# Kernel tuning notes

Measured on AMD Instinct MI355X. Metric: run time of the kernel, lower is better.

Reference implementation:

```python
import jax, jax.numpy as jnp
import numpy as np

VOCAB = 50257
EMBED = 256
UNITS = 1024   # dec_units == attention units == GRU units
ENC_D = 1024   # encoder feature dim
B = 64
T_ENC = 128


def setup_inputs() -> dict:
    key = jax.random.key(0)
    ks = jax.random.split(key, 16)
    s = lambda k, *sh: jax.random.normal(k, sh, dtype=jnp.float32) * 0.02
    gru_in = ENC_D + EMBED  # concat(context, embedding)
    return {
        "x": jax.random.randint(ks[0], (B, 1), 0, VOCAB),
        "hidden": jax.random.normal(ks[1], (B, UNITS), dtype=jnp.float32),
        "enc_output": jax.random.normal(ks[2], (B, T_ENC, ENC_D), dtype=jnp.float32),
        "emb": s(ks[3], VOCAB, EMBED),
        "W1": s(ks[4], UNITS, UNITS), "b1": jnp.zeros((UNITS,), jnp.float32),
        "W2": s(ks[5], ENC_D, UNITS), "b2": jnp.zeros((UNITS,), jnp.float32),
        "V": s(ks[6], UNITS, 1), "bV": jnp.zeros((1,), jnp.float32),
        "gru_kernel": s(ks[7], gru_in, 3 * UNITS),
        "gru_rkernel": s(ks[8], UNITS, 3 * UNITS),
        "gru_bias": jnp.zeros((2, 3 * UNITS), jnp.float32),  # reset_after=True: [input_bias, recurrent_bias]
        "fcW": s(ks[9], UNITS, VOCAB), "fcb": jnp.zeros((VOCAB,), jnp.float32),
    }


def reference(x, hidden, enc_output, emb, W1, b1, W2, b2, V, bV,
              gru_kernel, gru_rkernel, gru_bias, fcW, fcb):
    # --- Bahdanau attention ---
    q = hidden[:, None, :] @ W1 + b1                    # [B,1,U]
    k = enc_output @ W2 + b2                            # [B,T,U]
    score = jnp.tanh(q + k) @ V + bV                    # [B,T,1]
    attw = jax.nn.softmax(score, axis=1)                # [B,T,1]
    context = jnp.sum(attw * enc_output, axis=1)        # [B,ENC_D]

    # --- embed token and concat (single time step) ---
    e = emb[x[:, 0]]                                    # [B,EMBED]
    xin = jnp.concatenate([context, e], axis=-1)        # [B,ENC_D+EMBED]

    # --- single GRU step (keras default reset_after=True), initial state zeros
    # (original code calls self.gru(x) without initial_state) ---
    h0 = jnp.zeros((xin.shape[0], UNITS), xin.dtype)
    xz, xr, xh = jnp.split(xin @ gru_kernel + gru_bias[0], 3, axis=-1)
    rz, rr, rh = jnp.split(h0 @ gru_rkernel + gru_bias[1], 3, axis=-1)
    z = jax.nn.sigmoid(xz + rz)
    r = jax.nn.sigmoid(xr + rr)
    hh = jnp.tanh(xh + r * rh)
    h = z * h0 + (1.0 - z) * hh                          # [B,U]

    logits = h @ fcW + fcb                               # [B,VOCAB]
    return logits, h, attw
```

## Files before the change

kernel.cpp:

```cpp
#include <hip/hip_runtime.h>
#include <hip/hip_bf16.h>

#define UNITS 1024
#define EMBED 256
#define TENC  128
#define BATCH 64
#define VOCAB 50257
#define GRU_IN 1280
#define MROWS 8192
#define NCB   8
#define NSPLIT 8

typedef __bf16 bf16x8 __attribute__((ext_vector_type(8)));
typedef float  f32x4  __attribute__((ext_vector_type(4)));
typedef float  f32x4u __attribute__((ext_vector_type(4), aligned(4)));

__device__ __forceinline__ void gload_lds16(const void* gsrc, void* ldst) {
  __builtin_amdgcn_global_load_lds(
      (const __attribute__((address_space(1))) void*)gsrc,
      (__attribute__((address_space(3))) void*)ldst,
      16, 0, 0);
}

__global__ __launch_bounds__(256) void convert_kernel(
    const float* __restrict__ enc, const float* __restrict__ W2,
    __bf16* __restrict__ encb, __bf16* __restrict__ w2t)
{
  __shared__ __bf16 tl[64][72];
  const int bid = blockIdx.x;
  const int tid = threadIdx.x;
  if (bid < 4096) {
    const size_t base = ((size_t)bid * 256 + tid) * 8;
    const f32x4 v0 = *reinterpret_cast<const f32x4*>(enc + base);
    const f32x4 v1 = *reinterpret_cast<const f32x4*>(enc + base + 4);
    bf16x8 o;
#pragma unroll
    for (int j = 0; j < 4; ++j) { o[j] = (__bf16)v0[j]; o[4 + j] = (__bf16)v1[j]; }
    *reinterpret_cast<bf16x8*>(encb + base) = o;
  } else {
    const int ti  = bid - 4096;
    const int kt0 = (ti >> 4) * 64, nt0 = (ti & 15) * 64;
    const int r = tid >> 2, q = (tid & 3) * 16;
    const float* wp = W2 + (size_t)(kt0 + r) * UNITS + nt0 + q;
#pragma unroll
    for (int v = 0; v < 4; ++v) {
      const f32x4 a = *reinterpret_cast<const f32x4*>(wp + v * 4);
#pragma unroll
      for (int j = 0; j < 4; ++j) tl[r][q + v * 4 + j] = (__bf16)a[j];
    }
    __syncthreads();
    const int n = tid >> 2, kq = (tid & 3) * 16;
    bf16x8 o0, o1;
#pragma unroll
    for (int j = 0; j < 8; ++j) { o0[j] = tl[kq + j][n]; o1[j] = tl[kq + 8 + j][n]; }
    __bf16* op = w2t + (size_t)(nt0 + n) * UNITS + kt0 + kq;
    *reinterpret_cast<bf16x8*>(op)     = o0;
    *reinterpret_cast<bf16x8*>(op + 8) = o1;
  }
}

__global__ __launch_bounds__(256) void gemm_splitk(
    const float* __restrict__ A, const float* __restrict__ B,
    float* __restrict__ Cpart, int M, int N, int K, int Kc)
{
  const int col0  = blockIdx.y * 64;
  const int kbase = blockIdx.z * Kc;
  const int tid  = threadIdx.x;
  const int lane = tid & 63;
  const int wid  = tid >> 6;
  const int wm   = (wid >> 1) * 32;
  const int wn   = (wid & 1) * 32;

  __shared__ __bf16 As[2][4][64][8];
  __shared__ __bf16 Bs[2][4][64][8];

  f32x4 acc[2][2] = {};

  const int ar  = tid >> 2;
  const int akc = (tid & 3) * 8;
  const int bkk = tid >> 4;
  const int bn  = (tid & 15) * 4;

  f32x4 pa0[2], pa1[2], pb0[2], pb1[2];

  auto LOAD = [&](int k0, int s) {
    const float* ap = A + (size_t)ar * K + k0 + akc;
    pa0[s] = *reinterpret_cast<const f32x4*>(ap);
    pa1[s] = *reinterpret_cast<const f32x4*>(ap + 4);
    const float* bp0 = B + (size_t)(k0 + bkk) * N + col0 + bn;
    pb0[s] = *reinterpret_cast<const f32x4*>(bp0);
    pb1[s] = *reinterpret_cast<const f32x4*>(bp0 + (size_t)16 * N);
  };
  auto STAGE = [&](int s, int bb) {
    bf16x8 v;
#pragma unroll
    for (int j = 0; j < 4; ++j) { v[j] = (__bf16)pa0[s][j]; v[4 + j] = (__bf16)pa1[s][j]; }
    *reinterpret_cast<bf16x8*>(&As[bb][tid & 3][ar][0]) = v;
#pragma unroll
    for (int j = 0; j < 4; ++j) {
      Bs[bb][bkk >> 3][bn + j][bkk & 7]               = (__bf16)pb0[s][j];
      Bs[bb][(bkk + 16) >> 3][bn + j][(bkk + 16) & 7] = (__bf16)pb1[s][j];
    }
  };
  auto COMPUTE = [&](int bb) {
    bf16x8 af[2], bfr[2];
#pragma unroll
    for (int f = 0; f < 2; ++f) {
      af[f]  = *reinterpret_cast<const bf16x8*>(&As[bb][lane >> 4][wm + f * 16 + (lane & 15)][0]);
      bfr[f] = *reinterpret_cast<const bf16x8*>(&Bs[bb][lane >> 4][wn + f * 16 + (lane & 15)][0]);
    }
#pragma unroll
    for (int fm = 0; fm < 2; ++fm)
#pragma unroll
      for (int fn = 0; fn < 2; ++fn)
        acc[fm][fn] = __builtin_amdgcn_mfma_f32_16x16x32_bf16(af[fm], bfr[fn], acc[fm][fn], 0, 0, 0);
  };

  const int nt = Kc >> 5;
  LOAD(kbase, 0);
  LOAD(kbase + 32, 1);
  STAGE(0, 0);
  __syncthreads();
  for (int t = 0; t < nt; t += 2) {
    if (t + 2 < nt) LOAD(kbase + ((t + 2) << 5), 0);
    COMPUTE(0);
    if (t + 1 < nt) STAGE(1, 1);
    __syncthreads();
    if (t + 1 < nt) {
      if (t + 3 < nt) LOAD(kbase + ((t + 3) << 5), 1);
      COMPUTE(1);
      if (t + 2 < nt) STAGE(0, 0);
      __syncthreads();
    }
  }

  float* Cz = Cpart + (size_t)blockIdx.z * M * N;
#pragma unroll
  for (int fm = 0; fm < 2; ++fm) {
    const int rbase = wm + fm * 16 + (lane >> 4) * 4;
#pragma unroll
    for (int fn = 0; fn < 2; ++fn) {
      const int gc = col0 + wn + fn * 16 + (lane & 15);
#pragma unroll
      for (int r = 0; r < 4; ++r)
        Cz[(size_t)(rbase + r) * N + gc] = acc[fm][fn][r];
    }
  }
}

__global__ __launch_bounds__(256) void gemm_fc(
    const float* __restrict__ A, const float* __restrict__ B,
    const float* __restrict__ bias, float* __restrict__ C, int N)
{
  const int col0 = blockIdx.x * 64;
  const int tid  = threadIdx.x;
  const int lane = tid & 63;
  const int wid  = tid >> 6;
  const int wm   = (wid >> 1) * 32;
  const int wn   = (wid & 1) * 32;

  __shared__ __bf16 As[2][4][64][8];
  __shared__ __bf16 Bs[2][4][64][8];

  f32x4 acc[2][2] = {};

  const int ar  = tid >> 2;
  const int akc = (tid & 3) * 8;
  const int bkk = tid >> 4;
  const int bn  = (tid & 15) * 4;
  const int gn  = col0 + bn;
  const bool okb = (gn + 3 < N);

  f32x4 pa0[2], pa1[2], pb0[2], pb1[2];

  auto LOAD = [&](int k0, int s) {
    const float* ap = A + (size_t)ar * UNITS + k0 + akc;
    pa0[s] = *reinterpret_cast<const f32x4*>(ap);
    pa1[s] = *reinterpret_cast<const f32x4*>(ap + 4);
    const float* bp0 = B + (size_t)(k0 + bkk) * N + gn;
    const float* bp1 = bp0 + (size_t)16 * N;
    if (okb) {
      pb0[s] = *reinterpret_cast<const f32x4u*>(bp0);
      pb1[s] = *reinterpret_cast<const f32x4u*>(bp1);
    } else {
      f32x4 t0 = {0,0,0,0}, t1 = {0,0,0,0};
#pragma unroll
      for (int j = 0; j < 4; ++j)
        if (gn + j < N) { t0[j] = bp0[j]; t1[j] = bp1[j]; }
      pb0[s] = t0; pb1[s] = t1;
    }
  };
  auto STAGE = [&](int s, int bb) {
    bf16x8 v;
#pragma unroll
    for (int j = 0; j < 4; ++j) { v[j] = (__bf16)pa0[s][j]; v[4 + j] = (__bf16)pa1[s][j]; }
    *reinterpret_cast<bf16x8*>(&As[bb][tid & 3][ar][0]) = v;
#pragma unroll
    for (int j = 0; j < 4; ++j) {
      Bs[bb][bkk >> 3][bn + j][bkk & 7]               = (__bf16)pb0[s][j];
      Bs[bb][(bkk + 16) >> 3][bn + j][(bkk + 16) & 7] = (__bf16)pb1[s][j];
    }
  };
  auto COMPUTE = [&](int bb) {
    bf16x8 af[2], bfr[2];
#pragma unroll
    for (int f = 0; f < 2; ++f) {
      af[f]  = *reinterpret_cast<const bf16x8*>(&As[bb][lane >> 4][wm + f * 16 + (lane & 15)][0]);
      bfr[f] = *reinterpret_cast<const bf16x8*>(&Bs[bb][lane >> 4][wn + f * 16 + (lane & 15)][0]);
    }
#pragma unroll
    for (int fm = 0; fm < 2; ++fm)
#pragma unroll
      for (int fn = 0; fn < 2; ++fn)
        acc[fm][fn] = __builtin_amdgcn_mfma_f32_16x16x32_bf16(af[fm], bfr[fn], acc[fm][fn], 0, 0, 0);
  };

  LOAD(0, 0);
  LOAD(32, 1);
  STAGE(0, 0);
  __syncthreads();
#pragma unroll 1
  for (int t = 0; t < 32; t += 2) {
    if (t + 2 < 32) LOAD((t + 2) << 5, 0);
    COMPUTE(0);
    STAGE(1, 1);
    __syncthreads();
    if (t + 3 < 32) LOAD((t + 3) << 5, 1);
    COMPUTE(1);
    if (t + 2 < 32) STAGE(0, 0);
    __syncthreads();
  }

#pragma unroll
  for (int fm = 0; fm < 2; ++fm) {
    const int rbase = wm + fm * 16 + (lane >> 4) * 4;
#pragma unroll
    for (int fn = 0; fn < 2; ++fn) {
      const int gc = col0 + wn + fn * 16 + (lane & 15);
      if (gc >= N) continue;
      const float bv = bias[gc];
#pragma unroll
      for (int r = 0; r < 4; ++r)
        __builtin_nontemporal_store(acc[fm][fn][r] + bv, &C[(size_t)(rbase + r) * N + gc]);
    }
  }
}

__global__ __launch_bounds__(256) void k_score_mfma(
    const __bf16* __restrict__ encb, const __bf16* __restrict__ w2t,
    const float* __restrict__ b1, const float* __restrict__ b2,
    const float* __restrict__ qpart, const float* __restrict__ Vw,
    float* __restrict__ partial)
{
  const int b    = blockIdx.x;
  const int row0 = b * TENC;
  const int col0 = blockIdx.y * 128;
  const int tid  = threadIdx.x;
  const int lane = tid & 63;
  const int wid  = tid >> 6;
  const int wm   = (wid >> 1) * 64;
  const int wn   = (wid & 1) * 64;

  __shared__ __bf16 As[8][128][8];
  __shared__ __bf16 Bs[8][128][8];
  __shared__ float  sred[2][128];

  f32x4 acc[4][4] = {};

  for (int t = 0; t < 16; ++t) {
    const int k0 = t * 64;
#pragma unroll
    for (int j = 0; j < 4; ++j) {
      const int i  = wid * 4 + j;
      const int c  = i >> 1, rh = (i & 1) * 64;
      const __bf16* ga = encb + (size_t)(row0 + rh + lane) * UNITS + k0 + c * 8;
      gload_lds16(ga, &As[c][rh][0]);
      const __bf16* gb = w2t + (size_t)(col0 + rh + lane) * UNITS + k0 + c * 8;
      gload_lds16(gb, &Bs[c][rh][0]);
    }
    __syncthreads();

#pragma unroll
    for (int s = 0; s < 2; ++s) {
      bf16x8 af[4], bfr[4];
#pragma unroll
      for (int f = 0; f < 4; ++f) {
        af[f]  = *reinterpret_cast<const bf16x8*>(&As[s * 4 + (lane >> 4)][wm + f * 16 + (lane & 15)][0]);
        bfr[f] = *reinterpret_cast<const bf16x8*>(&Bs[s * 4 + (lane >> 4)][wn + f * 16 + (lane & 15)][0]);
      }
#pragma unroll
      for (int fm = 0; fm < 4; ++fm)
#pragma unroll
        for (int fn = 0; fn < 4; ++fn)
          acc[fm][fn] = __builtin_amdgcn_mfma_f32_16x16x32_bf16(af[fm], bfr[fn], acc[fm][fn], 0, 0, 0);
    }
    __syncthreads();
  }

  float rowsum[4][4] = {};
#pragma unroll
  for (int fn = 0; fn < 4; ++fn) {
    const int gc = col0 + wn + fn * 16 + (lane & 15);
    float qv = b1[gc] + b2[gc];
#pragma unroll
    for (int s = 0; s < NSPLIT; ++s)
      qv += qpart[(size_t)s * BATCH * UNITS + (size_t)b * UNITS + gc];
    const float vv = Vw[gc];
#pragma unroll
    for (int fm = 0; fm < 4; ++fm)
#pragma unroll
      for (int r = 0; r < 4; ++r)
        rowsum[fm][r] += tanhf(qv + acc[fm][fn][r]) * vv;
  }
#pragma unroll
  for (int off = 8; off; off >>= 1)
#pragma unroll
    for (int fm = 0; fm < 4; ++fm)
#pragma unroll
      for (int r = 0; r < 4; ++r)
        rowsum[fm][r] += __shfl_xor(rowsum[fm][r], off);
  if ((lane & 15) == 0) {
#pragma unroll
    for (int fm = 0; fm < 4; ++fm)
#pragma unroll
      for (int r = 0; r < 4; ++r)
        sred[wid & 1][wm + fm * 16 + (lane >> 4) * 4 + r] = rowsum[fm][r];
  }
  __syncthreads();
  if (tid < TENC)
    partial[(size_t)blockIdx.y * MROWS + row0 + tid] = sred[0][tid] + sred[1][tid];
}

__global__ __launch_bounds__(256) void ctx_kernel(
    const float* __restrict__ enc, const float* __restrict__ partial,
    const float* __restrict__ bV, const float* __restrict__ emb,
    const int* __restrict__ x, float* __restrict__ attw,
    float* __restrict__ xin)
{
  const int b   = blockIdx.x;
  const int tid = threadIdx.x;
  __shared__ float scs[TENC];
  __shared__ float red[4];

  if (tid < TENC) {
    float s = bV[0];
#pragma unroll
    for (int cb = 0; cb < NCB; ++cb) s += partial[(size_t)cb * MROWS + b * TENC + tid];
    float m = s;
#pragma unroll
    for (int off = 32; off; off >>= 1) m = fmaxf(m, __shfl_xor(m, off));
    if ((tid & 63) == 0) red[tid >> 6] = m;
    scs[tid] = s;
  }
  __syncthreads();
  const float mm = fmaxf(red[0], red[1]);
  if (tid < TENC) {
    const float e = expf(scs[tid] - mm);
    scs[tid] = e;
    float su = e;
#pragma unroll
    for (int off = 32; off; off >>= 1) su += __shfl_xor(su, off);
    if ((tid & 63) == 0) red[2 + (tid >> 6)] = su;
  }
  __syncthreads();
  const float inv = 1.f / (red[2] + red[3]);
  if (tid < TENC) scs[tid] *= inv;
  __syncthreads();

  if (blockIdx.y == 0 && tid < TENC) attw[(size_t)b * TENC + tid] = scs[tid];

  const int n = blockIdx.y * 256 + tid;
  const float* ep = enc + (size_t)b * TENC * UNITS + n;
  float c = 0.f;
#pragma unroll 8
  for (int t = 0; t < TENC; ++t) c += scs[t] * ep[(size_t)t * UNITS];
  xin[(size_t)b * GRU_IN + n] = c;
  if (blockIdx.y == 0)
    xin[(size_t)b * GRU_IN + UNITS + tid] = emb[(size_t)x[b] * EMBED + tid];
}

__global__ __launch_bounds__(256) void gru_pw(
    const float* __restrict__ gpart, const float* __restrict__ gb0,
    const float* __restrict__ gb1, float* __restrict__ h)
{
  const int i = blockIdx.x * 256 + threadIdx.x;
  const int b = i >> 10, n = i & 1023;
  float xz = gb0[n], xr = gb0[1024 + n], xh = gb0[2048 + n];
#pragma unroll
  for (int s = 0; s < NSPLIT; ++s) {
    const float* g = gpart + (size_t)s * BATCH * 3072 + (size_t)b * 3072;
    xz += g[n]; xr += g[1024 + n]; xh += g[2048 + n];
  }
  const float rz = gb1[n], rr = gb1[1024 + n], rh = gb1[2048 + n];
  const float z = 1.f / (1.f + expf(-(xz + rz)));
  const float r = 1.f / (1.f + expf(-(xr + rr)));
  const float hh = tanhf(xh + r * rh);
  h[i] = (1.f - z) * hh;
}

extern "C" void kernel_launch(void* const* d_in, const int* in_sizes, int n_in,
                              void* d_out, int out_size, void* d_ws, size_t ws_size,
                              hipStream_t stream)
{
  (void)in_sizes; (void)n_in; (void)out_size; (void)ws_size;
  const int*   x      = (const int*)  d_in[0];
  const float* hidden = (const float*)d_in[1];
  const float* enc    = (const float*)d_in[2];
  const float* emb    = (const float*)d_in[3];
  const float* W1     = (const float*)d_in[4];
  const float* b1     = (const float*)d_in[5];
  const float* W2     = (const float*)d_in[6];
  const float* b2     = (const float*)d_in[7];
  const float* Vw     = (const float*)d_in[8];
  const float* bV     = (const float*)d_in[9];
  const float* gk     = (const float*)d_in[10];
  const float* gb     = (const float*)d_in[12];
  const float* fcW    = (const float*)d_in[13];
  const float* fcb    = (const float*)d_in[14];

  float* ws      = (float*)d_ws;
  float* qpart   = ws;
  float* partial = qpart + 524288;
  float* xin     = partial + 65536;
  float* gpart   = xin + 81920;
  __bf16* encb   = (__bf16*)(gpart + 1572864);
  __bf16* w2t    = encb + (size_t)MROWS * UNITS;

  float* out    = (float*)d_out;
  float* logits = out;
  float* hout   = out + (size_t)BATCH * VOCAB;
  float* attw   = hout + BATCH * UNITS;

  hipLaunchKernelGGL(convert_kernel, dim3(4096 + 256), dim3(256), 0, stream,
                     enc, W2, encb, w2t);
  hipLaunchKernelGGL(gemm_splitk, dim3(1, 16, NSPLIT), dim3(256), 0, stream,
                     hidden, W1, qpart, 64, 1024, 1024, 128);
  hipLaunchKernelGGL(k_score_mfma, dim3(64, NCB), dim3(256), 0, stream,
                     encb, w2t, b1, b2, qpart, Vw, partial);
  hipLaunchKernelGGL(ctx_kernel, dim3(64, 4), dim3(256), 0, stream,
                     enc, partial, bV, emb, x, attw, xin);
  hipLaunchKernelGGL(gemm_splitk, dim3(1, 48, NSPLIT), dim3(256), 0, stream,
                     xin, gk, gpart, 64, 3072, 1280, 160);
  hipLaunchKernelGGL(gru_pw, dim3(256), dim3(256), 0, stream,
                     gpart, gb, gb + 3072, hout);
  hipLaunchKernelGGL(gemm_fc, dim3((VOCAB + 63) / 64), dim3(256), 0, stream,
                     hout, fcW, fcb, logits, VOCAB);
}
```

Before: 146.2 us.

## Fuse query GEMM into prep, widen FC tile, double-buffer score GEMM, split ctx

Merges the hidden@W1 split-K GEMM into the bf16 conversion launch to save a kernel launch. Widens the vocab projection GEMM tile to 128 columns so each block reuses the A tile over more columns. Adds LDS double buffering to the attention-score MFMA kernel so global-to-LDS loads overlap compute. Splits the context reduction over time into four groups with more blocks for parallelism. The trade-offs are more LDS and register use per block and fewer FC blocks.

```diff
diff --git a/kernel.cpp b/kernel.cpp
--- a/kernel.cpp
+++ b/kernel.cpp
@@ -22,13 +22,18 @@
       16, 0, 0);
 }
 
-__global__ __launch_bounds__(256) void convert_kernel(
+__global__ __launch_bounds__(256) void prep_kernel(
     const float* __restrict__ enc, const float* __restrict__ W2,
-    __bf16* __restrict__ encb, __bf16* __restrict__ w2t)
+    const float* __restrict__ hidden, const float* __restrict__ W1,
+    __bf16* __restrict__ encb, __bf16* __restrict__ w2t,
+    float* __restrict__ qpart)
 {
   __shared__ __bf16 tl[64][72];
+  __shared__ __bf16 As[2][4][64][8];
+  __shared__ __bf16 Bs[2][4][64][8];
   const int bid = blockIdx.x;
   const int tid = threadIdx.x;
+
   if (bid < 4096) {
     const size_t base = ((size_t)bid * 256 + tid) * 8;
     const f32x4 v0 = *reinterpret_cast<const f32x4*>(enc + base);
@@ -37,7 +42,9 @@
 #pragma unroll
     for (int j = 0; j < 4; ++j) { o[j] = (__bf16)v0[j]; o[4 + j] = (__bf16)v1[j]; }
     *reinterpret_cast<bf16x8*>(encb + base) = o;
-  } else {
+    return;
+  }
+  if (bid < 4352) {
     const int ti  = bid - 4096;
     const int kt0 = (ti >> 4) * 64, nt0 = (ti & 15) * 64;
     const int r = tid >> 2, q = (tid & 3) * 16;
@@ -56,6 +63,84 @@
     __bf16* op = w2t + (size_t)(nt0 + n) * UNITS + kt0 + kq;
     *reinterpret_cast<bf16x8*>(op)     = o0;
     *reinterpret_cast<bf16x8*>(op + 8) = o1;
+    return;
+  }
+
+  const int idx   = bid - 4352;
+  const int col0  = (idx & 15) * 64;
+  const int kbase = (idx >> 4) * 128;
+  const int lane = tid & 63;
+  const int wid  = tid >> 6;
+  const int wm   = (wid >> 1) * 32;
+  const int wn   = (wid & 1) * 32;
+
+  f32x4 acc[2][2] = {};
+  const int ar  = tid >> 2;
+  const int akc = (tid & 3) * 8;
+  const int bkk = tid >> 4;
+  const int bn  = (tid & 15) * 4;
+
+  f32x4 pa0[2], pa1[2], pb0[2], pb1[2];
+  auto LOAD = [&](int k0, int s) {
+    const float* ap = hidden + (size_t)ar * UNITS + k0 + akc;
+    pa0[s] = *reinterpret_cast<const f32x4*>(ap);
+    pa1[s] = *reinterpret_cast<const f32x4*>(ap + 4);
+    const float* bp0 = W1 + (size_t)(k0 + bkk) * UNITS + col0 + bn;
+    pb0[s] = *reinterpret_cast<const f32x4*>(bp0);
+    pb1[s] = *reinterpret_cast<const f32x4*>(bp0 + (size_t)16 * UNITS);
+  };
+  auto STAGE = [&](int s, int bb) {
+    bf16x8 v;
+#pragma unroll
+    for (int j = 0; j < 4; ++j) { v[j] = (__bf16)pa0[s][j]; v[4 + j] = (__bf16)pa1[s][j]; }
+    *reinterpret_cast<bf16x8*>(&As[bb][tid & 3][ar][0]) = v;
+#pragma unroll
+    for (int j = 0; j < 4; ++j) {
+      Bs[bb][bkk >> 3][bn + j][bkk & 7]               = (__bf16)pb0[s][j];
+      Bs[bb][(bkk + 16) >> 3][bn + j][(bkk + 16) & 7] = (__bf16)pb1[s][j];
+    }
+  };
+  auto COMPUTE = [&](int bb) {
+    bf16x8 af[2], bfr[2];
+#pragma unroll
+    for (int f = 0; f < 2; ++f) {
+      af[f]  = *reinterpret_cast<const bf16x8*>(&As[bb][lane >> 4][wm + f * 16 + (lane & 15)][0]);
+      bfr[f] = *reinterpret_cast<const bf16x8*>(&Bs[bb][lane >> 4][wn + f * 16 + (lane & 15)][0]);
+    }
+#pragma unroll
+    for (int fm = 0; fm < 2; ++fm)
+#pragma unroll
+      for (int fn = 0; fn < 2; ++fn)
+        acc[fm][fn] = __builtin_amdgcn_mfma_f32_16x16x32_bf16(af[fm], bfr[fn], acc[fm][fn], 0, 0, 0);
+  };
+
+  LOAD(kbase, 0);
+  LOAD(kbase + 32, 1);
+  STAGE(0, 0);
+  __syncthreads();
+#pragma unroll 1
+  for (int t = 0; t < 4; t += 2) {
+    if (t + 2 < 4) LOAD(kbase + ((t + 2) << 5), 0);
+    COMPUTE(0);
+    STAGE(1, 1);
+    __syncthreads();
+    if (t + 3 < 4) LOAD(kbase + ((t + 3) << 5), 1);
+    COMPUTE(1);
+    if (t + 2 < 4) STAGE(0, 0);
+    __syncthreads();
+  }
+
+  float* Cz = qpart + (size_t)(idx >> 4) * BATCH * UNITS;
+#pragma unroll
+  for (int fm = 0; fm < 2; ++fm) {
+    const int rbase = wm + fm * 16 + (lane >> 4) * 4;
+#pragma unroll
+    for (int fn = 0; fn < 2; ++fn) {
+      const int gc = col0 + wn + fn * 16 + (lane & 15);
+#pragma unroll
+      for (int r = 0; r < 4; ++r)
+        Cz[(size_t)(rbase + r) * UNITS + gc] = acc[fm][fn][r];
+    }
   }
 }
 
@@ -152,43 +237,47 @@
     const float* __restrict__ A, const float* __restrict__ B,
     const float* __restrict__ bias, float* __restrict__ C, int N)
 {
-  const int col0 = blockIdx.x * 64;
+  const int col0 = blockIdx.x * 128;
   const int tid  = threadIdx.x;
   const int lane = tid & 63;
   const int wid  = tid >> 6;
   const int wm   = (wid >> 1) * 32;
-  const int wn   = (wid & 1) * 32;
+  const int wn   = (wid & 1) * 64;
 
   __shared__ __bf16 As[2][4][64][8];
-  __shared__ __bf16 Bs[2][4][64][8];
-
-  f32x4 acc[2][2] = {};
+  __shared__ __bf16 Bs[2][4][128][8];
+
+  f32x4 acc[2][4] = {};
 
   const int ar  = tid >> 2;
   const int akc = (tid & 3) * 8;
   const int bkk = tid >> 4;
-  const int bn  = (tid & 15) * 4;
+  const int bn  = (tid & 15) * 8;
   const int gn  = col0 + bn;
-  const bool okb = (gn + 3 < N);
-
-  f32x4 pa0[2], pa1[2], pb0[2], pb1[2];
-
+
+  f32x4 pb[2][4];
+  f32x4 pa0[2], pa1[2];
+
+  auto LD8 = [&](const float* p, f32x4& a, f32x4& b) {
+    if (gn + 7 < N) {
+      a = *reinterpret_cast<const f32x4u*>(p);
+      b = *reinterpret_cast<const f32x4u*>(p + 4);
+    } else {
+      a = (f32x4){0,0,0,0}; b = (f32x4){0,0,0,0};
+#pragma unroll
+      for (int j = 0; j < 4; ++j) {
+        if (gn + j < N)     a[j] = p[j];
+        if (gn + 4 + j < N) b[j] = p[4 + j];
+      }
+    }
+  };
   auto LOAD = [&](int k0, int s) {
     const float* ap = A + (size_t)ar * UNITS + k0 + akc;
     pa0[s] = *reinterpret_cast<const f32x4*>(ap);
     pa1[s] = *reinterpret_cast<const f32x4*>(ap + 4);
     const float* bp0 = B + (size_t)(k0 + bkk) * N + gn;
-    const float* bp1 = bp0 + (size_t)16 * N;
-    if (okb) {
-      pb0[s] = *reinterpret_cast<const f32x4u*>(bp0);
-      pb1[s] = *reinterpret_cast<const f32x4u*>(bp1);
-    } else {
-      f32x4 t0 = {0,0,0,0}, t1 = {0,0,0,0};
-#pragma unroll
-      for (int j = 0; j < 4; ++j)
-        if (gn + j < N) { t0[j] = bp0[j]; t1[j] = bp1[j]; }
-      pb0[s] = t0; pb1[s] = t1;
-    }
+    LD8(bp0, pb[s][0], pb[s][1]);
+    LD8(bp0 + (size_t)16 * N, pb[s][2], pb[s][3]);
   };
   auto STAGE = [&](int s, int bb) {
     bf16x8 v;
@@ -196,22 +285,25 @@
     for (int j = 0; j < 4; ++j) { v[j] = (__bf16)pa0[s][j]; v[4 + j] = (__bf16)pa1[s][j]; }
     *reinterpret_cast<bf16x8*>(&As[bb][tid & 3][ar][0]) = v;
 #pragma unroll
-    for (int j = 0; j < 4; ++j) {
-      Bs[bb][bkk >> 3][bn + j][bkk & 7]               = (__bf16)pb0[s][j];
-      Bs[bb][(bkk + 16) >> 3][bn + j][(bkk + 16) & 7] = (__bf16)pb1[s][j];
+    for (int j = 0; j < 8; ++j) {
+      const float lo = (j < 4) ? pb[s][0][j] : pb[s][1][j - 4];
+      const float hi = (j < 4) ? pb[s][2][j] : pb[s][3][j - 4];
+      Bs[bb][bkk >> 3][bn + j][bkk & 7]               = (__bf16)lo;
+      Bs[bb][(bkk + 16) >> 3][bn + j][(bkk + 16) & 7] = (__bf16)hi;
     }
   };
   auto COMPUTE = [&](int bb) {
-    bf16x8 af[2], bfr[2];
-#pragma unroll
-    for (int f = 0; f < 2; ++f) {
-      af[f]  = *reinterpret_cast<const bf16x8*>(&As[bb][lane >> 4][wm + f * 16 + (lane & 15)][0]);
+    bf16x8 af[2], bfr[4];
+#pragma unroll
+    for (int f = 0; f < 2; ++f)
+      af[f] = *reinterpret_cast<const bf16x8*>(&As[bb][lane >> 4][wm + f * 16 + (lane & 15)][0]);
+#pragma unroll
+    for (int f = 0; f < 4; ++f)
       bfr[f] = *reinterpret_cast<const bf16x8*>(&Bs[bb][lane >> 4][wn + f * 16 + (lane & 15)][0]);
-    }
 #pragma unroll
     for (int fm = 0; fm < 2; ++fm)
 #pragma unroll
-      for (int fn = 0; fn < 2; ++fn)
+      for (int fn = 0; fn < 4; ++fn)
         acc[fm][fn] = __builtin_amdgcn_mfma_f32_16x16x32_bf16(af[fm], bfr[fn], acc[fm][fn], 0, 0, 0);
   };
 
@@ -235,7 +327,7 @@
   for (int fm = 0; fm < 2; ++fm) {
     const int rbase = wm + fm * 16 + (lane >> 4) * 4;
 #pragma unroll
-    for (int fn = 0; fn < 2; ++fn) {
+    for (int fn = 0; fn < 4; ++fn) {
       const int gc = col0 + wn + fn * 16 + (lane & 15);
       if (gc >= N) continue;
       const float bv = bias[gc];
@@ -261,32 +353,36 @@
   const int wm   = (wid >> 1) * 64;
   const int wn   = (wid & 1) * 64;
 
-  __shared__ __bf16 As[8][128][8];
-  __shared__ __bf16 Bs[8][128][8];
+  __shared__ __bf16 As[2][8][128][8];
+  __shared__ __bf16 Bs[2][8][128][8];
   __shared__ float  sred[2][128];
 
   f32x4 acc[4][4] = {};
 
-  for (int t = 0; t < 16; ++t) {
+  auto STAGE = [&](int t, int bb) {
     const int k0 = t * 64;
 #pragma unroll
     for (int j = 0; j < 4; ++j) {
       const int i  = wid * 4 + j;
       const int c  = i >> 1, rh = (i & 1) * 64;
-      const __bf16* ga = encb + (size_t)(row0 + rh + lane) * UNITS + k0 + c * 8;
-      gload_lds16(ga, &As[c][rh][0]);
-      const __bf16* gb = w2t + (size_t)(col0 + rh + lane) * UNITS + k0 + c * 8;
-      gload_lds16(gb, &Bs[c][rh][0]);
-    }
-    __syncthreads();
-
+      gload_lds16(encb + (size_t)(row0 + rh + lane) * UNITS + k0 + c * 8, &As[bb][c][rh][0]);
+      gload_lds16(w2t  + (size_t)(col0 + rh + lane) * UNITS + k0 + c * 8, &Bs[bb][c][rh][0]);
+    }
+  };
+
+  STAGE(0, 0);
+  __syncthreads();
+  int cur = 0;
+#pragma unroll 1
+  for (int t = 0; t < 16; ++t) {
+    if (t + 1 < 16) STAGE(t + 1, cur ^ 1);
 #pragma unroll
     for (int s = 0; s < 2; ++s) {
       bf16x8 af[4], bfr[4];
 #pragma unroll
       for (int f = 0; f < 4; ++f) {
-        af[f]  = *reinterpret_cast<const bf16x8*>(&As[s * 4 + (lane >> 4)][wm + f * 16 + (lane & 15)][0]);
-        bfr[f] = *reinterpret_cast<const bf16x8*>(&Bs[s * 4 + (lane >> 4)][wn + f * 16 + (lane & 15)][0]);
+        af[f]  = *reinterpret_cast<const bf16x8*>(&As[cur][s * 4 + (lane >> 4)][wm + f * 16 + (lane & 15)][0]);
+        bfr[f] = *reinterpret_cast<const bf16x8*>(&Bs[cur][s * 4 + (lane >> 4)][wn + f * 16 + (lane & 15)][0]);
       }
 #pragma unroll
       for (int fm = 0; fm < 4; ++fm)
@@ -295,6 +391,7 @@
           acc[fm][fn] = __builtin_amdgcn_mfma_f32_16x16x32_bf16(af[fm], bfr[fn], acc[fm][fn], 0, 0, 0);
     }
     __syncthreads();
+    cur ^= 1;
   }
 
   float rowsum[4][4] = {};
@@ -338,9 +435,13 @@
     float* __restrict__ xin)
 {
   const int b   = blockIdx.x;
+  const int yb  = blockIdx.y;
   const int tid = threadIdx.x;
+  const int g   = tid >> 6;
+  const int n   = tid & 63;
   __shared__ float scs[TENC];
   __shared__ float red[4];
+  __shared__ float csum[4][64];
 
   if (tid < TENC) {
     float s = bV[0];
@@ -364,18 +465,20 @@
   }
   __syncthreads();
   const float inv = 1.f / (red[2] + red[3]);
-  if (tid < TENC) scs[tid] *= inv;
-  __syncthreads();
-
-  if (blockIdx.y == 0 && tid < TENC) attw[(size_t)b * TENC + tid] = scs[tid];
-
-  const int n = blockIdx.y * 256 + tid;
-  const float* ep = enc + (size_t)b * TENC * UNITS + n;
+
+  if (yb == 0 && tid < TENC) attw[(size_t)b * TENC + tid] = scs[tid] * inv;
+
+  const int n0 = yb * 64;
+  const float* ep = enc + ((size_t)b * TENC + g * 32) * UNITS + n0 + n;
   float c = 0.f;
 #pragma unroll 8
-  for (int t = 0; t < TENC; ++t) c += scs[t] * ep[(size_t)t * UNITS];
-  xin[(size_t)b * GRU_IN + n] = c;
-  if (blockIdx.y == 0)
+  for (int i = 0; i < 32; ++i) c += scs[g * 32 + i] * ep[(size_t)i * UNITS];
+  csum[g][n] = c;
+  __syncthreads();
+  if (tid < 64)
+    xin[(size_t)b * GRU_IN + n0 + tid] =
+        (csum[0][tid] + csum[1][tid] + csum[2][tid] + csum[3][tid]) * inv;
+  if (yb == 0)
     xin[(size_t)b * GRU_IN + UNITS + tid] = emb[(size_t)x[b] * EMBED + tid];
 }
 
@@ -431,18 +534,16 @@
   float* hout   = out + (size_t)BATCH * VOCAB;
   float* attw   = hout + BATCH * UNITS;
 
-  hipLaunchKernelGGL(convert_kernel, dim3(4096 + 256), dim3(256), 0, stream,
-                     enc, W2, encb, w2t);
-  hipLaunchKernelGGL(gemm_splitk, dim3(1, 16, NSPLIT), dim3(256), 0, stream,
-                     hidden, W1, qpart, 64, 1024, 1024, 128);
+  hipLaunchKernelGGL(prep_kernel, dim3(4096 + 256 + 128), dim3(256), 0, stream,
+                     enc, W2, hidden, W1, encb, w2t, qpart);
   hipLaunchKernelGGL(k_score_mfma, dim3(64, NCB), dim3(256), 0, stream,
                      encb, w2t, b1, b2, qpart, Vw, partial);
-  hipLaunchKernelGGL(ctx_kernel, dim3(64, 4), dim3(256), 0, stream,
+  hipLaunchKernelGGL(ctx_kernel, dim3(64, 16), dim3(256), 0, stream,
                      enc, partial, bV, emb, x, attw, xin);
   hipLaunchKernelGGL(gemm_splitk, dim3(1, 48, NSPLIT), dim3(256), 0, stream,
                      xin, gk, gpart, 64, 3072, 1280, 160);
   hipLaunchKernelGGL(gru_pw, dim3(256), dim3(256), 0, stream,
                      gpart, gb, gb + 3072, hout);
-  hipLaunchKernelGGL(gemm_fc, dim3((VOCAB + 63) / 64), dim3(256), 0, stream,
+  hipLaunchKernelGGL(gemm_fc, dim3((VOCAB + 127) / 128), dim3(256), 0, stream,
                      hout, fcW, fcb, logits, VOCAB);
 }
```

After: 179.8 us. 1.23x slower.
